# Kernel optimization log

Hardware: AMD Instinct MI355X
Metric: run time of the kernel (lower is better)

## Reference

```python
import jax, jax.numpy as jnp
import numpy as np

N_NODES = 256
COND = 64
ARCH = [256, 512, 1024]
E = N_NODES * (N_NODES - 1) // 2  # 32640 upper-triangular edges
OUT = 2 * E                        # 65280 final-layer width
B = 512
CUTOFF = 0.0
TAU = 1.0


def _make_params(key, dims):
    ws, bs = [], []
    for i, (din, dout) in enumerate(zip(dims[:-1], dims[1:])):
        k = jax.random.fold_in(key, i)
        kw, kb = jax.random.split(k)
        ws.append(jax.random.normal(kw, (din, dout), jnp.float32) * 0.02)
        bs.append(jax.random.normal(kb, (dout,), jnp.float32) * 0.02)
    return ws, bs


def setup_inputs() -> dict:
    key = jax.random.key(0)
    kx, kg, kbig, ksmall = jax.random.split(key, 4)
    x = jax.random.normal(kx, (B, COND), jnp.float32)
    gumbel = jax.random.gumbel(kg, (B, E, 2), jnp.float32)
    dims = [COND] + ARCH + [OUT]
    bw, bb = _make_params(kbig, dims)
    sw, sb = _make_params(ksmall, dims)
    inp = {"x": x, "gumbel": gumbel}
    for i in range(4):
        inp[f"bw{i}"] = bw[i]; inp[f"bb{i}"] = bb[i]
        inp[f"sw{i}"] = sw[i]; inp[f"sb{i}"] = sb[i]
    return inp


def _expert_adj(x, ws, bs, gumbel):
    # MLP: relu on all but last layer
    h = x
    for w, b in zip(ws[:-1], bs[:-1]):
        h = jax.nn.relu(h @ w + b)
    logits = (h @ ws[-1] + bs[-1]).reshape(x.shape[0], E, 2)
    # hard gumbel-softmax (straight-through), tau=1
    g = (logits + gumbel) / TAU
    y_soft = jax.nn.softmax(g, axis=-1)
    y_hard = jax.nn.one_hot(jnp.argmax(g, axis=-1), 2, dtype=y_soft.dtype)
    y = y_hard + y_soft - jax.lax.stop_gradient(y_soft)
    x0 = y[:, :, 0]  # [B, E]
    iu, ju = jnp.triu_indices(N_NODES, k=1)
    adj = jnp.zeros((x.shape[0], N_NODES, N_NODES), x0.dtype)
    adj = adj.at[:, iu, ju].set(x0)
    return adj + jnp.swapaxes(adj, 1, 2)


def reference(x, gumbel,
              bw0, bb0, bw1, bb1, bw2, bb2, bw3, bb3,
              sw0, sb0, sw1, sb1, sw2, sb2, sw3, sb3):
    big_ws, big_bs = [bw0, bw1, bw2, bw3], [bb0, bb1, bb2, bb3]
    small_ws, small_bs = [sw0, sw1, sw2, sw3], [sb0, sb1, sb2, sb3]
    adj_big = _expert_adj(x, big_ws, big_bs, gumbel)
    adj_small = _expert_adj(x, small_ws, small_bs, gumbel)
    mask_big = x[:, 0] > CUTOFF  # [B]
    out = jnp.where(mask_big[:, None, None], adj_big, adj_small)
    return out
```

## Files before the change

### kernel.cpp

```cpp
#include <hip/hip_runtime.h>

#define N_NODES 256
#define COND    64
#define E_PAIRS 32640
#define OUTCOLS 65280
#define BATCH   512
#define SLOTS   576
#define D1      256
#define D2      512
#define D3      1024

typedef __attribute__((ext_vector_type(8))) short bf16x8;
typedef __attribute__((ext_vector_type(4))) float f32x4;
typedef __attribute__((ext_vector_type(4))) unsigned int u32x4;

static __device__ __forceinline__ unsigned short f2bf(float f) {
    unsigned int u = __float_as_uint(f);
    u += 0x7FFF + ((u >> 16) & 1);
    return (unsigned short)(u >> 16);
}
static __device__ __forceinline__ float bf2f(unsigned short h) {
    return __uint_as_float(((unsigned int)h) << 16);
}

__global__ void k0_sort(const float* __restrict__ x, int* __restrict__ meta,
                        int* __restrict__ borig) {
    __shared__ int wc[9];
    int t = threadIdx.x;
    if (t < SLOTS) borig[t] = -1;
    int m = 0;
    if (t < BATCH) m = (x[t * COND] > 0.0f) ? 1 : 0;
    unsigned long long bm = __ballot(m);
    int wave = t >> 6;
    int lane = t & 63;
    int lanePre = __popcll(bm & ((1ull << lane) - 1ull));
    if (lane == 0) wc[wave] = __popcll(bm);
    __syncthreads();
    int nbig = 0, preBig = 0;
    #pragma unroll
    for (int w = 0; w < 8; ++w) {
        int c = wc[w];
        if (w < wave) preBig += c;
        nbig += c;
    }
    int S = (nbig + 63) & ~63;
    if (t < BATCH) {
        int onesBefore = preBig + lanePre;
        int slot = m ? onesBefore : (S + (t - onesBefore));
        borig[slot] = t;
    }
    if (t == 0) meta[0] = S;
}

template <bool GATHER, int K, int DOUT, bool SPLIT>
__global__ __launch_bounds__(256) void k1_gemm(
    const float* __restrict__ in,
    const float* __restrict__ wbig, const float* __restrict__ bbig,
    const float* __restrict__ wsml, const float* __restrict__ bsml,
    const int* __restrict__ meta, const int* __restrict__ borig,
    float* __restrict__ out, unsigned short* __restrict__ hbA) {
    __shared__ float hs[16][64 + 4];
    __shared__ float wt[16][64 + 4];
    int tid = threadIdx.x;
    int by = blockIdx.x;
    int bx = blockIdx.y;
    int r0 = by * 64;
    int cb = bx * 64;
    int S = meta[0];
    bool big = (r0 < S);
    const float* w = big ? wbig : wsml;
    const float* bias = big ? bbig : bsml;

    int lm = tid >> 2;
    int lq = tid & 3;
    int wk = tid >> 4;
    int wc = (tid & 15) * 4;

    int tm = tid >> 4;
    int tn = tid & 15;

    const float* hrow;
    if (GATHER) {
        int b = borig[r0 + lm];
        hrow = (b >= 0) ? &in[(size_t)b * K] : (const float*)0;
    } else {
        hrow = &in[(size_t)(r0 + lm) * K];
    }

    float acc[4][4];
    #pragma unroll
    for (int i = 0; i < 4; ++i)
        #pragma unroll
        for (int j = 0; j < 4; ++j) acc[i][j] = 0.f;

    for (int k0 = 0; k0 < K; k0 += 16) {
        float4 hv = make_float4(0.f, 0.f, 0.f, 0.f);
        if (!GATHER || hrow) hv = *(const float4*)&hrow[k0 + lq * 4];
        float4 wv = *(const float4*)&w[(size_t)(k0 + wk) * DOUT + cb + wc];
        __syncthreads();
        hs[lq * 4 + 0][lm] = hv.x;
        hs[lq * 4 + 1][lm] = hv.y;
        hs[lq * 4 + 2][lm] = hv.z;
        hs[lq * 4 + 3][lm] = hv.w;
        *(float4*)&wt[wk][wc] = wv;
        __syncthreads();
        #pragma unroll
        for (int kk = 0; kk < 16; ++kk) {
            float4 a  = *(const float4*)&hs[kk][tm * 4];
            float4 bf = *(const float4*)&wt[kk][tn * 4];
            acc[0][0] = fmaf(a.x, bf.x, acc[0][0]);
            acc[0][1] = fmaf(a.x, bf.y, acc[0][1]);
            acc[0][2] = fmaf(a.x, bf.z, acc[0][2]);
            acc[0][3] = fmaf(a.x, bf.w, acc[0][3]);
            acc[1][0] = fmaf(a.y, bf.x, acc[1][0]);
            acc[1][1] = fmaf(a.y, bf.y, acc[1][1]);
            acc[1][2] = fmaf(a.y, bf.z, acc[1][2]);
            acc[1][3] = fmaf(a.y, bf.w, acc[1][3]);
            acc[2][0] = fmaf(a.z, bf.x, acc[2][0]);
            acc[2][1] = fmaf(a.z, bf.y, acc[2][1]);
            acc[2][2] = fmaf(a.z, bf.z, acc[2][2]);
            acc[2][3] = fmaf(a.z, bf.w, acc[2][3]);
            acc[3][0] = fmaf(a.w, bf.x, acc[3][0]);
            acc[3][1] = fmaf(a.w, bf.y, acc[3][1]);
            acc[3][2] = fmaf(a.w, bf.z, acc[3][2]);
            acc[3][3] = fmaf(a.w, bf.w, acc[3][3]);
        }
    }

    float4 bv = *(const float4*)&bias[cb + tn * 4];
    #pragma unroll
    for (int i = 0; i < 4; ++i) {
        float o[4];
        o[0] = fmaxf(acc[i][0] + bv.x, 0.f);
        o[1] = fmaxf(acc[i][1] + bv.y, 0.f);
        o[2] = fmaxf(acc[i][2] + bv.z, 0.f);
        o[3] = fmaxf(acc[i][3] + bv.w, 0.f);
        if (SPLIT) {
            int row = r0 + tm * 4 + i;
            int by_ = row >> 6, rl = row & 63;
            int mfr = rl >> 4, p15 = rl & 15;
            int kt  = cb + tn * 4;
            int kk  = kt >> 5, lgk = (kt >> 3) & 3, j0 = kt & 7;
            size_t base = (size_t)(by_ * 32 + kk) * 6144 + (size_t)mfr * 512
                        + (size_t)(lgk * 16 + p15) * 8 + j0;
            ushort4 s0, s1, s2;
            unsigned short* q0[4] = {&s0.x, &s0.y, &s0.z, &s0.w};
            unsigned short* q1[4] = {&s1.x, &s1.y, &s1.z, &s1.w};
            unsigned short* q2[4] = {&s2.x, &s2.y, &s2.z, &s2.w};
            #pragma unroll
            for (int j = 0; j < 4; ++j) {
                unsigned short a0 = f2bf(o[j]);
                float r1v = o[j] - bf2f(a0);
                unsigned short a1 = f2bf(r1v);
                float r2v = r1v - bf2f(a1);
                *q0[j] = a0; *q1[j] = a1; *q2[j] = f2bf(r2v);
            }
            *(ushort4*)&hbA[base]        = s0;
            *(ushort4*)&hbA[base + 2048] = s1;
            *(ushort4*)&hbA[base + 4096] = s2;
        } else {
            float4 ov;
            ov.x = o[0]; ov.y = o[1]; ov.z = o[2]; ov.w = o[3];
            *(float4*)&out[(size_t)(r0 + tm * 4 + i) * DOUT + cb + tn * 4] = ov;
        }
    }
}

__global__ __launch_bounds__(256, 3) void k2_mfma(
    const unsigned short* __restrict__ hbA,
    const float* __restrict__ bw3, const float* __restrict__ bb3,
    const float* __restrict__ sw3, const float* __restrict__ sb3,
    const float* __restrict__ gum,
    const int* __restrict__ meta, const int* __restrict__ borig,
    unsigned char* __restrict__ bits) {
    int tid = threadIdx.x;
    int wgid = blockIdx.x;
    int xr  = wgid & 7;
    int s_  = wgid >> 3;
    int by  = s_ % 9;
    int q   = s_ / 9;
    int bx  = q * 8 + xr;
    if (bx >= 255) return;

    int r0 = by * 64;
    int db = bx * 128;
    int S = meta[0];
    bool big = (r0 < S);
    const float* w3 = big ? bw3 : sw3;
    const float* b3 = big ? bb3 : sb3;

    int lane = tid & 63;
    int wid  = tid >> 6;
    int l15  = lane & 15;
    int lg   = lane >> 4;

    int colg0 = db + wid * 32 + l15;

    f32x4 acc[4][2];
    #pragma unroll
    for (int m = 0; m < 4; ++m)
        #pragma unroll
        for (int n = 0; n < 2; ++n) acc[m][n] = (f32x4)0.f;

    const unsigned short* ap0 = hbA + (size_t)(by * 32) * 6144 + (size_t)lane * 8;
    const float* wbase = w3 + (size_t)(lg * 8) * OUTCOLS + 2 * (size_t)colg0;

#define LOADB(BUF, KK) do {                                                     \
    const float* wp_ = wbase + (size_t)(KK) * 32 * OUTCOLS;                     \
    _Pragma("unroll")                                                           \
    for (int n_ = 0; n_ < 2; ++n_) {                                            \
        _Pragma("unroll")                                                       \
        for (int j_ = 0; j_ < 8; ++j_)                                          \
            BUF[n_ * 8 + j_] = *(const float2*)(wp_ + (size_t)j_ * OUTCOLS      \
                                                + n_ * 32);                     \
    }                                                                           \
} while (0)

#define STEP(BUF, KK) do {                                                      \
    const unsigned short* ap_ = ap0 + (size_t)(KK) * 6144;                      \
    bf16x8 af_[3][4];                                                           \
    _Pragma("unroll")                                                           \
    for (int l_ = 0; l_ < 3; ++l_)                                              \
        _Pragma("unroll")                                                       \
        for (int m_ = 0; m_ < 4; ++m_)                                          \
            af_[l_][m_] = *(const bf16x8*)(ap_ + l_ * 2048 + m_ * 512);         \
    _Pragma("unroll")                                                           \
    for (int n_ = 0; n_ < 2; ++n_) {                                            \
        u32x4 f0_, f1_, f2_;                                                    \
        _Pragma("unroll")                                                       \
        for (int w_ = 0; w_ < 4; ++w_) {                                        \
            float dA_ = BUF[n_ * 8 + 2 * w_].x     - BUF[n_ * 8 + 2 * w_].y;    \
            float dB_ = BUF[n_ * 8 + 2 * w_ + 1].x - BUF[n_ * 8 + 2 * w_ + 1].y;\
            unsigned short aL_ = f2bf(dA_), aH_ = f2bf(dB_);                    \
            f0_[w_] = (unsigned int)aL_ | ((unsigned int)aH_ << 16);            \
            float rA_ = dA_ - bf2f(aL_), rB_ = dB_ - bf2f(aH_);                 \
            unsigned short bL_ = f2bf(rA_), bH_ = f2bf(rB_);                    \
            f1_[w_] = (unsigned int)bL_ | ((unsigned int)bH_ << 16);            \
            float sA_ = rA_ - bf2f(bL_), sB_ = rB_ - bf2f(bH_);                 \
            f2_[w_] = (unsigned int)f2bf(sA_) | ((unsigned int)f2bf(sB_) << 16);\
        }                                                                       \
        bf16x8 b0_ = __builtin_bit_cast(bf16x8, f0_);                           \
        bf16x8 b1_ = __builtin_bit_cast(bf16x8, f1_);                           \
        bf16x8 b2_ = __builtin_bit_cast(bf16x8, f2_);                           \
        _Pragma("unroll")                                                       \
        for (int m_ = 0; m_ < 4; ++m_) {                                        \
            f32x4 c_ = acc[m_][n_];                                             \
            c_ = __builtin_amdgcn_mfma_f32_16x16x32_bf16(af_[0][m_], b0_, c_, 0, 0, 0); \
            c_ = __builtin_amdgcn_mfma_f32_16x16x32_bf16(af_[0][m_], b1_, c_, 0, 0, 0); \
            c_ = __builtin_amdgcn_mfma_f32_16x16x32_bf16(af_[1][m_], b0_, c_, 0, 0, 0); \
            c_ = __builtin_amdgcn_mfma_f32_16x16x32_bf16(af_[1][m_], b1_, c_, 0, 0, 0); \
            c_ = __builtin_amdgcn_mfma_f32_16x16x32_bf16(af_[0][m_], b2_, c_, 0, 0, 0); \
            c_ = __builtin_amdgcn_mfma_f32_16x16x32_bf16(af_[2][m_], b0_, c_, 0, 0, 0); \
            acc[m_][n_] = c_;                                                   \
        }                                                                       \
    }                                                                           \
} while (0)

    float2 brE[16], brO[16];
    LOADB(brE, 0);
    for (int ki = 0; ki < 16; ++ki) {
        int ke = ki * 2;
        LOADB(brO, ke + 1);
        STEP(brE, ke);
        LOADB(brE, (ki < 15) ? ke + 2 : 31);
        STEP(brO, ke + 1);
    }
#undef LOADB
#undef STEP

    #pragma unroll
    for (int n = 0; n < 2; ++n) {
        int colg = db + wid * 32 + n * 16 + l15;
        float2 bv = *(const float2*)&b3[2 * colg];
        float bd = bv.x - bv.y;
        #pragma unroll
        for (int m = 0; m < 4; ++m) {
            #pragma unroll
            for (int r = 0; r < 4; ++r) {
                int slot = r0 + m * 16 + lg * 4 + r;
                int b = borig[slot];
                if (b < 0) continue;
                float2 gv = *(const float2*)&gum[(size_t)b * OUTCOLS + 2 * colg];
                float g = acc[m][n][r] + bd + (gv.x - gv.y);
                bits[(size_t)b * E_PAIRS + colg] = (g >= 0.f) ? 1 : 0;
            }
        }
    }
}

__global__ __launch_bounds__(256) void k3_expand(
    const unsigned char* __restrict__ bits, float* __restrict__ out) {
    __shared__ unsigned char L[64][68];
    const int ti_tab[10] = {0,0,0,0,1,1,1,2,2,3};
    const int tj_tab[10] = {0,1,2,3,1,2,3,2,3,3};
    int p = blockIdx.x;
    int b = blockIdx.y;
    int ti = ti_tab[p], tj = tj_tab[p];
    int t = threadIdx.x;

    {
        int r = t >> 2;
        int q = t & 3;
        int i = ti * 64 + r;
        long base = (long)b * E_PAIRS + (long)i * (511 - i) / 2 - i - 1;
        int j0 = tj * 64 + q * 16;
        #pragma unroll
        for (int k = 0; k < 16; ++k) {
            int j = j0 + k;
            unsigned char v = (j > i) ? bits[base + j] : (unsigned char)0;
            L[r][q * 16 + k] = v;
        }
    }
    __syncthreads();

    int h  = t >> 4;
    int w4 = (t & 15) * 4;

    {
        #pragma unroll
        for (int rr = 0; rr < 4; ++rr) {
            int ii = rr * 16 + h;
            int i_ = ti * 64 + ii;
            float4 v;
            if (ti == tj) {
                int jj;
                jj = w4 + 0; v.x = (jj > ii) ? (float)L[ii][jj] : (jj < ii ? (float)L[jj][ii] : 0.f);
                jj = w4 + 1; v.y = (jj > ii) ? (float)L[ii][jj] : (jj < ii ? (float)L[jj][ii] : 0.f);
                jj = w4 + 2; v.z = (jj > ii) ? (float)L[ii][jj] : (jj < ii ? (float)L[jj][ii] : 0.f);
                jj = w4 + 3; v.w = (jj > ii) ? (float)L[ii][jj] : (jj < ii ? (float)L[jj][ii] : 0.f);
            } else {
                v.x = (float)L[ii][w4 + 0];
                v.y = (float)L[ii][w4 + 1];
                v.z = (float)L[ii][w4 + 2];
                v.w = (float)L[ii][w4 + 3];
            }
            size_t o = (((size_t)b * 256 + i_) * 256) + tj * 64 + w4;
            *(float4*)&out[o] = v;
        }
    }

    if (ti != tj) {
        #pragma unroll
        for (int rr = 0; rr < 4; ++rr) {
            int jj = rr * 16 + h;
            int j_ = tj * 64 + jj;
            float4 v;
            v.x = (float)L[w4 + 0][jj];
            v.y = (float)L[w4 + 1][jj];
            v.z = (float)L[w4 + 2][jj];
            v.w = (float)L[w4 + 3][jj];
            size_t o = (((size_t)b * 256 + j_) * 256) + ti * 64 + w4;
            *(float4*)&out[o] = v;
        }
    }
}

extern "C" void kernel_launch(void* const* d_in, const int* in_sizes, int n_in,
                              void* d_out, int out_size, void* d_ws, size_t ws_size,
                              hipStream_t stream) {
    const float* x   = (const float*)d_in[0];
    const float* gum = (const float*)d_in[1];
    const float* bw0 = (const float*)d_in[2];  const float* bb0 = (const float*)d_in[3];
    const float* sw0 = (const float*)d_in[4];  const float* sb0 = (const float*)d_in[5];
    const float* bw1 = (const float*)d_in[6];  const float* bb1 = (const float*)d_in[7];
    const float* sw1 = (const float*)d_in[8];  const float* sb1 = (const float*)d_in[9];
    const float* bw2 = (const float*)d_in[10]; const float* bb2 = (const float*)d_in[11];
    const float* sw2 = (const float*)d_in[12]; const float* sb2 = (const float*)d_in[13];
    const float* bw3 = (const float*)d_in[14]; const float* bb3 = (const float*)d_in[15];
    const float* sw3 = (const float*)d_in[16]; const float* sb3 = (const float*)d_in[17];

    char* ws = (char*)d_ws;
    int*   meta  = (int*)ws;
    int*   borig = (int*)(ws + 64);
    float* act1  = (float*)(ws + 4096);
    float* act2  = (float*)(ws + 593920);
    unsigned short* hbA = (unsigned short*)(ws + 1773568);
    unsigned char* bits = (unsigned char*)(ws + 5312512);
    float* out = (float*)d_out;

    k0_sort<<<1, SLOTS, 0, stream>>>(x, meta, borig);
    k1_gemm<true,  COND, D1, false><<<dim3(9, D1 / 64), 256, 0, stream>>>(
        x,    bw0, bb0, sw0, sb0, meta, borig, act1, 0);
    k1_gemm<false, D1,   D2, false><<<dim3(9, D2 / 64), 256, 0, stream>>>(
        act1, bw1, bb1, sw1, sb1, meta, borig, act2, 0);
    k1_gemm<false, D2,   D3, true><<<dim3(9, D3 / 64), 256, 0, stream>>>(
        act2, bw2, bb2, sw2, sb2, meta, borig, (float*)0, hbA);
    k2_mfma<<<2304, 256, 0, stream>>>(hbA, bw3, bb3, sw3, sb3, gum,
                                      meta, borig, bits);
    k3_expand<<<dim3(10, BATCH), 256, 0, stream>>>(bits, out);
}
```

Baseline: 992.9 us.

## Stage final-layer weight tiles through LDS with async global-to-LDS loads

The last-layer MFMA kernel now copies each 32x256 fp32 weight tile into a double-buffered shared-memory array using global_load_lds with 16-byte coalesced row loads. Previously each lane fetched strided float2 pieces straight into registers. Each wave then reads its fragments from LDS and forms the three-way bf16 split as before, with a block barrier between stages. The per-block occupancy hint is dropped. The 64 KB LDS footprint per block caps residency, the strided LDS reads may hit bank conflicts, and correctness depends on the async LDS writes being complete before the barrier.

```diff
diff --git a/kernel.cpp b/kernel.cpp
--- a/kernel.cpp
+++ b/kernel.cpp
@@ -21,6 +21,13 @@
 }
 static __device__ __forceinline__ float bf2f(unsigned short h) {
     return __uint_as_float(((unsigned int)h) << 16);
+}
+
+static __device__ __forceinline__ void gload_lds16(const float* g, float* l) {
+    __builtin_amdgcn_global_load_lds(
+        (const __attribute__((address_space(1))) unsigned int*)g,
+        (__attribute__((address_space(3))) unsigned int*)l,
+        16, 0, 0);
 }
 
 __global__ void k0_sort(const float* __restrict__ x, int* __restrict__ meta,
@@ -166,13 +173,15 @@
     }
 }
 
-__global__ __launch_bounds__(256, 3) void k2_mfma(
+__global__ __launch_bounds__(256) void k2_mfma(
     const unsigned short* __restrict__ hbA,
     const float* __restrict__ bw3, const float* __restrict__ bb3,
     const float* __restrict__ sw3, const float* __restrict__ sb3,
     const float* __restrict__ gum,
     const int* __restrict__ meta, const int* __restrict__ borig,
     unsigned char* __restrict__ bits) {
+    __shared__ float Braw[2][32][256];
+
     int tid = threadIdx.x;
     int wgid = blockIdx.x;
     int xr  = wgid & 7;
@@ -183,6 +192,7 @@
     if (bx >= 255) return;
 
     int r0 = by * 64;
+    int cb = bx * 256;
     int db = bx * 128;
     int S = meta[0];
     bool big = (r0 < S);
@@ -194,8 +204,6 @@
     int l15  = lane & 15;
     int lg   = lane >> 4;
 
-    int colg0 = db + wid * 32 + l15;
-
     f32x4 acc[4][2];
     #pragma unroll
     for (int m = 0; m < 4; ++m)
@@ -203,21 +211,19 @@
         for (int n = 0; n < 2; ++n) acc[m][n] = (f32x4)0.f;
 
     const unsigned short* ap0 = hbA + (size_t)(by * 32) * 6144 + (size_t)lane * 8;
-    const float* wbase = w3 + (size_t)(lg * 8) * OUTCOLS + 2 * (size_t)colg0;
-
-#define LOADB(BUF, KK) do {                                                     \
-    const float* wp_ = wbase + (size_t)(KK) * 32 * OUTCOLS;                     \
+    const float* wtile = w3 + cb;
+
+#define STAGE(BUF, T) do {                                                      \
     _Pragma("unroll")                                                           \
-    for (int n_ = 0; n_ < 2; ++n_) {                                            \
-        _Pragma("unroll")                                                       \
-        for (int j_ = 0; j_ < 8; ++j_)                                          \
-            BUF[n_ * 8 + j_] = *(const float2*)(wp_ + (size_t)j_ * OUTCOLS      \
-                                                + n_ * 32);                     \
+    for (int rr_ = 0; rr_ < 8; ++rr_) {                                         \
+        int row_ = wid * 8 + rr_;                                               \
+        gload_lds16(wtile + (size_t)((T) * 32 + row_) * OUTCOLS + lane * 4,     \
+                    &Braw[BUF][row_][0]);                                       \
     }                                                                           \
 } while (0)
 
-#define STEP(BUF, KK) do {                                                      \
-    const unsigned short* ap_ = ap0 + (size_t)(KK) * 6144;                      \
+#define STEP(BUF, T) do {                                                       \
+    const unsigned short* ap_ = ap0 + (size_t)(T) * 6144;                       \
     bf16x8 af_[3][4];                                                           \
     _Pragma("unroll")                                                           \
     for (int l_ = 0; l_ < 3; ++l_)                                              \
@@ -226,11 +232,14 @@
             af_[l_][m_] = *(const bf16x8*)(ap_ + l_ * 2048 + m_ * 512);         \
     _Pragma("unroll")                                                           \
     for (int n_ = 0; n_ < 2; ++n_) {                                            \
+        int fi_ = wid * 64 + n_ * 32 + l15 * 2;  \
         u32x4 f0_, f1_, f2_;                                                    \
         _Pragma("unroll")                                                       \
         for (int w_ = 0; w_ < 4; ++w_) {                                        \
-            float dA_ = BUF[n_ * 8 + 2 * w_].x     - BUF[n_ * 8 + 2 * w_].y;    \
-            float dB_ = BUF[n_ * 8 + 2 * w_ + 1].x - BUF[n_ * 8 + 2 * w_ + 1].y;\
+            float2 pA_ = *(const float2*)&Braw[BUF][lg * 8 + 2 * w_][fi_];      \
+            float2 pB_ = *(const float2*)&Braw[BUF][lg * 8 + 2 * w_ + 1][fi_];  \
+            float dA_ = pA_.x - pA_.y;                                          \
+            float dB_ = pB_.x - pB_.y;                                          \
             unsigned short aL_ = f2bf(dA_), aH_ = f2bf(dB_);                    \
             f0_[w_] = (unsigned int)aL_ | ((unsigned int)aH_ << 16);            \
             float rA_ = dA_ - bf2f(aL_), rB_ = dB_ - bf2f(aH_);                 \
@@ -256,16 +265,15 @@
     }                                                                           \
 } while (0)
 
-    float2 brE[16], brO[16];
-    LOADB(brE, 0);
-    for (int ki = 0; ki < 16; ++ki) {
-        int ke = ki * 2;
-        LOADB(brO, ke + 1);
-        STEP(brE, ke);
-        LOADB(brE, (ki < 15) ? ke + 2 : 31);
-        STEP(brO, ke + 1);
-    }
-#undef LOADB
+    STAGE(0, 0);
+    __syncthreads();
+    for (int t = 0; t < 32; ++t) {
+        int buf = t & 1;
+        if (t < 31) STAGE(buf ^ 1, t + 1);
+        STEP(buf, t);
+        __syncthreads();
+    }
+#undef STAGE
 #undef STEP
 
     #pragma unroll
```

After: 1.070 ms. 7.8% more time.

## Retile final-layer MFMA so each weight split feeds three row blocks

Applied to the files above, without the earlier changes.

The final-layer kernel now gives each workgroup 64 columns and three 64-row batch blocks, not 128 columns and one row block. Each fp32 weight slice is loaded and split into three bf16 parts once, then reused across up to three row blocks. Big and small expert weights are only loaded when needed. This cuts repeated weight traffic and split arithmetic but drops the software double-buffering and the occupancy hint, and the grid shrinks to 1536 blocks, which may expose load latency.

```diff
diff --git a/kernel.cpp b/kernel.cpp
--- a/kernel.cpp
+++ b/kernel.cpp
@@ -166,7 +166,7 @@
     }
 }
 
-__global__ __launch_bounds__(256, 3) void k2_mfma(
+__global__ __launch_bounds__(256) void k2_mfma(
     const unsigned short* __restrict__ hbA,
     const float* __restrict__ bw3, const float* __restrict__ bb3,
     const float* __restrict__ sw3, const float* __restrict__ sb3,
@@ -175,114 +175,116 @@
     unsigned char* __restrict__ bits) {
     int tid = threadIdx.x;
     int wgid = blockIdx.x;
-    int xr  = wgid & 7;
-    int s_  = wgid >> 3;
-    int by  = s_ % 9;
-    int q   = s_ / 9;
-    int bx  = q * 8 + xr;
-    if (bx >= 255) return;
-
-    int r0 = by * 64;
-    int db = bx * 128;
-    int S = meta[0];
-    bool big = (r0 < S);
-    const float* w3 = big ? bw3 : sw3;
-    const float* b3 = big ? bb3 : sb3;
+    int r8   = wgid & 7;
+    int s_   = wgid >> 3;
+    int unit = r8 * 192 + s_;
+    if (unit >= 1530) return;
+    int c = unit / 3;
+    int g = unit % 3;
 
     int lane = tid & 63;
     int wid  = tid >> 6;
     int l15  = lane & 15;
     int lg   = lane >> 4;
 
-    int colg0 = db + wid * 32 + l15;
-
-    f32x4 acc[4][2];
-    #pragma unroll
-    for (int m = 0; m < 4; ++m)
-        #pragma unroll
-        for (int n = 0; n < 2; ++n) acc[m][n] = (f32x4)0.f;
-
-    const unsigned short* ap0 = hbA + (size_t)(by * 32) * 6144 + (size_t)lane * 8;
-    const float* wbase = w3 + (size_t)(lg * 8) * OUTCOLS + 2 * (size_t)colg0;
-
-#define LOADB(BUF, KK) do {                                                     \
-    const float* wp_ = wbase + (size_t)(KK) * 32 * OUTCOLS;                     \
+    int colg = c * 64 + wid * 16 + l15;
+    int S    = meta[0];
+    int nbt  = S >> 6;
+    int by0  = 3 * g;
+    bool big0 = (by0     < nbt);
+    bool big1 = (by0 + 1 < nbt);
+    bool big2 = (by0 + 2 < nbt);
+    bool needB = big0;
+    bool needS = !big2;
+
+    f32x4 acc[3][4];
+    #pragma unroll
+    for (int i = 0; i < 3; ++i)
+        #pragma unroll
+        for (int m = 0; m < 4; ++m) acc[i][m] = (f32x4)0.f;
+
+    bf16x8 Bb0 = {}, Bb1 = {}, Bb2 = {};
+    bf16x8 Bs0 = {}, Bs1 = {}, Bs2 = {};
+
+    const float* wbp = bw3 + 2 * (size_t)colg;
+    const float* wsp = sw3 + 2 * (size_t)colg;
+    const unsigned short* apbase = hbA + (size_t)lane * 8;
+
+#define SPLIT8(B0, B1, B2, WP) do {                                             \
+    u32x4 f0_, f1_, f2_;                                                        \
     _Pragma("unroll")                                                           \
-    for (int n_ = 0; n_ < 2; ++n_) {                                            \
-        _Pragma("unroll")                                                       \
-        for (int j_ = 0; j_ < 8; ++j_)                                          \
-            BUF[n_ * 8 + j_] = *(const float2*)(wp_ + (size_t)j_ * OUTCOLS      \
-                                                + n_ * 32);                     \
+    for (int p_ = 0; p_ < 4; ++p_) {                                            \
+        float2 pA_ = *(const float2*)((WP) + (size_t)(2 * p_) * OUTCOLS);       \
+        float2 pB_ = *(const float2*)((WP) + (size_t)(2 * p_ + 1) * OUTCOLS);   \
+        float dA_ = pA_.x - pA_.y, dB_ = pB_.x - pB_.y;                         \
+        unsigned short aL_ = f2bf(dA_), aH_ = f2bf(dB_);                        \
+        f0_[p_] = (unsigned)aL_ | ((unsigned)aH_ << 16);                        \
+        float rA_ = dA_ - bf2f(aL_), rB_ = dB_ - bf2f(aH_);                     \
+        unsigned short bL_ = f2bf(rA_), bH_ = f2bf(rB_);                        \
+        f1_[p_] = (unsigned)bL_ | ((unsigned)bH_ << 16);                        \
+        float sA_ = rA_ - bf2f(bL_), sB_ = rB_ - bf2f(bH_);                     \
+        f2_[p_] = (unsigned)f2bf(sA_) | ((unsigned)f2bf(sB_) << 16);            \
     }                                                                           \
+    B0 = __builtin_bit_cast(bf16x8, f0_);                                       \
+    B1 = __builtin_bit_cast(bf16x8, f1_);                                       \
+    B2 = __builtin_bit_cast(bf16x8, f2_);                                       \
 } while (0)
 
-#define STEP(BUF, KK) do {                                                      \
-    const unsigned short* ap_ = ap0 + (size_t)(KK) * 6144;                      \
+#define MMBODY(I, B0, B1, B2) do {                                              \
+    _Pragma("unroll") for (int m_ = 0; m_ < 4; ++m_)                            \
+        acc[I][m_] = __builtin_amdgcn_mfma_f32_16x16x32_bf16(af_[0][m_], B0, acc[I][m_], 0, 0, 0); \
+    _Pragma("unroll") for (int m_ = 0; m_ < 4; ++m_)                            \
+        acc[I][m_] = __builtin_amdgcn_mfma_f32_16x16x32_bf16(af_[0][m_], B1, acc[I][m_], 0, 0, 0); \
+    _Pragma("unroll") for (int m_ = 0; m_ < 4; ++m_)                            \
+        acc[I][m_] = __builtin_amdgcn_mfma_f32_16x16x32_bf16(af_[1][m_], B0, acc[I][m_], 0, 0, 0); \
+    _Pragma("unroll") for (int m_ = 0; m_ < 4; ++m_)                            \
+        acc[I][m_] = __builtin_amdgcn_mfma_f32_16x16x32_bf16(af_[1][m_], B1, acc[I][m_], 0, 0, 0); \
+    _Pragma("unroll") for (int m_ = 0; m_ < 4; ++m_)                            \
+        acc[I][m_] = __builtin_amdgcn_mfma_f32_16x16x32_bf16(af_[0][m_], B2, acc[I][m_], 0, 0, 0); \
+    _Pragma("unroll") for (int m_ = 0; m_ < 4; ++m_)                            \
+        acc[I][m_] = __builtin_amdgcn_mfma_f32_16x16x32_bf16(af_[2][m_], B0, acc[I][m_], 0, 0, 0); \
+} while (0)
+
+#define MM(I, ISBIG) do {                                                       \
+    const unsigned short* ap_ = apbase + (size_t)((by0 + (I)) * 32 + t) * 6144; \
     bf16x8 af_[3][4];                                                           \
-    _Pragma("unroll")                                                           \
-    for (int l_ = 0; l_ < 3; ++l_)                                              \
-        _Pragma("unroll")                                                       \
-        for (int m_ = 0; m_ < 4; ++m_)                                          \
+    _Pragma("unroll") for (int l_ = 0; l_ < 3; ++l_)                            \
+        _Pragma("unroll") for (int m_ = 0; m_ < 4; ++m_)                        \
             af_[l_][m_] = *(const bf16x8*)(ap_ + l_ * 2048 + m_ * 512);         \
-    _Pragma("unroll")                                                           \
-    for (int n_ = 0; n_ < 2; ++n_) {                                            \
-        u32x4 f0_, f1_, f2_;                                                    \
-        _Pragma("unroll")                                                       \
-        for (int w_ = 0; w_ < 4; ++w_) {                                        \
-            float dA_ = BUF[n_ * 8 + 2 * w_].x     - BUF[n_ * 8 + 2 * w_].y;    \
-            float dB_ = BUF[n_ * 8 + 2 * w_ + 1].x - BUF[n_ * 8 + 2 * w_ + 1].y;\
-            unsigned short aL_ = f2bf(dA_), aH_ = f2bf(dB_);                    \
-            f0_[w_] = (unsigned int)aL_ | ((unsigned int)aH_ << 16);            \
-            float rA_ = dA_ - bf2f(aL_), rB_ = dB_ - bf2f(aH_);                 \
-            unsigned short bL_ = f2bf(rA_), bH_ = f2bf(rB_);                    \
-            f1_[w_] = (unsigned int)bL_ | ((unsigned int)bH_ << 16);            \
-            float sA_ = rA_ - bf2f(bL_), sB_ = rB_ - bf2f(bH_);                 \
-            f2_[w_] = (unsigned int)f2bf(sA_) | ((unsigned int)f2bf(sB_) << 16);\
-        }                                                                       \
-        bf16x8 b0_ = __builtin_bit_cast(bf16x8, f0_);                           \
-        bf16x8 b1_ = __builtin_bit_cast(bf16x8, f1_);                           \
-        bf16x8 b2_ = __builtin_bit_cast(bf16x8, f2_);                           \
-        _Pragma("unroll")                                                       \
-        for (int m_ = 0; m_ < 4; ++m_) {                                        \
-            f32x4 c_ = acc[m_][n_];                                             \
-            c_ = __builtin_amdgcn_mfma_f32_16x16x32_bf16(af_[0][m_], b0_, c_, 0, 0, 0); \
-            c_ = __builtin_amdgcn_mfma_f32_16x16x32_bf16(af_[0][m_], b1_, c_, 0, 0, 0); \
-            c_ = __builtin_amdgcn_mfma_f32_16x16x32_bf16(af_[1][m_], b0_, c_, 0, 0, 0); \
-            c_ = __builtin_amdgcn_mfma_f32_16x16x32_bf16(af_[1][m_], b1_, c_, 0, 0, 0); \
-            c_ = __builtin_amdgcn_mfma_f32_16x16x32_bf16(af_[0][m_], b2_, c_, 0, 0, 0); \
-            c_ = __builtin_amdgcn_mfma_f32_16x16x32_bf16(af_[2][m_], b0_, c_, 0, 0, 0); \
-            acc[m_][n_] = c_;                                                   \
-        }                                                                       \
-    }                                                                           \
+    if (ISBIG) { MMBODY(I, Bb0, Bb1, Bb2); }                                    \
+    else       { MMBODY(I, Bs0, Bs1, Bs2); }                                    \
 } while (0)
 
-    float2 brE[16], brO[16];
-    LOADB(brE, 0);
-    for (int ki = 0; ki < 16; ++ki) {
-        int ke = ki * 2;
-        LOADB(brO, ke + 1);
-        STEP(brE, ke);
-        LOADB(brE, (ki < 15) ? ke + 2 : 31);
-        STEP(brO, ke + 1);
-    }
-#undef LOADB
-#undef STEP
-
-    #pragma unroll
-    for (int n = 0; n < 2; ++n) {
-        int colg = db + wid * 32 + n * 16 + l15;
-        float2 bv = *(const float2*)&b3[2 * colg];
-        float bd = bv.x - bv.y;
+    for (int t = 0; t < 32; ++t) {
+        size_t krow = (size_t)(t * 32 + lg * 8) * OUTCOLS;
+        if (needB) SPLIT8(Bb0, Bb1, Bb2, wbp + krow);
+        if (needS) SPLIT8(Bs0, Bs1, Bs2, wsp + krow);
+        MM(0, big0);
+        MM(1, big1);
+        MM(2, big2);
+    }
+#undef SPLIT8
+#undef MMBODY
+#undef MM
+
+    float2 bvB = *(const float2*)&bb3[2 * colg];
+    float2 bvS = *(const float2*)&sb3[2 * colg];
+    float bdB = bvB.x - bvB.y;
+    float bdS = bvS.x - bvS.y;
+    #pragma unroll
+    for (int i = 0; i < 3; ++i) {
+        int by = by0 + i;
+        float bd = (by < nbt) ? bdB : bdS;
         #pragma unroll
         for (int m = 0; m < 4; ++m) {
             #pragma unroll
             for (int r = 0; r < 4; ++r) {
-                int slot = r0 + m * 16 + lg * 4 + r;
+                int slot = by * 64 + m * 16 + lg * 4 + r;
                 int b = borig[slot];
                 if (b < 0) continue;
                 float2 gv = *(const float2*)&gum[(size_t)b * OUTCOLS + 2 * colg];
-                float g = acc[m][n][r] + bd + (gv.x - gv.y);
-                bits[(size_t)b * E_PAIRS + colg] = (g >= 0.f) ? 1 : 0;
+                float gval = acc[i][m][r] + bd + (gv.x - gv.y);
+                bits[(size_t)b * E_PAIRS + colg] = (gval >= 0.f) ? 1 : 0;
             }
         }
     }
@@ -385,7 +387,7 @@
         act1, bw1, bb1, sw1, sb1, meta, borig, act2, 0);
     k1_gemm<false, D2,   D3, true><<<dim3(9, D3 / 64), 256, 0, stream>>>(
         act2, bw2, bb2, sw2, sb2, meta, borig, (float*)0, hbA);
-    k2_mfma<<<2304, 256, 0, stream>>>(hbA, bw3, bb3, sw3, sb3, gum,
+    k2_mfma<<<1536, 256, 0, stream>>>(hbA, bw3, bb3, sw3, sb3, gum,
                                       meta, borig, bits);
     k3_expand<<<dim3(10, BATCH), 256, 0, stream>>>(bits, out);
 }
```

After: 1.147 ms. 15.6% more time.
